# Performance work log

Measured on AMD Instinct MI355X. Metric: run time of the kernel, lower is better.

## Reference

```python
import jax, jax.numpy as jnp
import numpy as np

B, T, C = 4, 2048, 1024
N_HEADS = 16
HEAD_DIM = C // N_HEADS

def setup_inputs() -> dict:
    key = jax.random.key(0)
    k1, k2, k3 = jax.random.split(key, 3)
    x = jax.random.normal(k1, (B, T, C), dtype=jnp.float32)
    w_attn = jax.random.normal(k2, (C, 3 * C), dtype=jnp.float32) * (1.0 / np.sqrt(C))
    b_attn = jnp.zeros((3 * C,), dtype=jnp.float32)
    w_proj = jax.random.normal(k3, (C, C), dtype=jnp.float32) * (1.0 / np.sqrt(C))
    b_proj = jnp.zeros((C,), dtype=jnp.float32)
    return {"x": x, "w_attn": w_attn, "b_attn": b_attn, "w_proj": w_proj, "b_proj": b_proj}

def reference(x, w_attn, b_attn, w_proj, b_proj):
    Bx, Tx, Cx = x.shape
    qkv = x @ w_attn + b_attn                      # [B,T,3C]
    q, k, v = jnp.split(qkv, 3, axis=-1)
    def heads(t):
        return t.reshape(Bx, Tx, N_HEADS, HEAD_DIM).transpose(0, 2, 1, 3)  # [B,H,T,D]
    q, k, v = heads(q), heads(k), heads(v)
    scale = 1.0 / np.sqrt(HEAD_DIM)
    attn = jnp.einsum('bhqd,bhkd->bhqk', q, k) * scale  # [B,H,T,T]
    causal = jnp.tril(jnp.ones((Tx, Tx), dtype=bool))
    attn = jnp.where(causal[None, None, :, :], attn, -jnp.inf)
    attn = jax.nn.softmax(attn, axis=-1)
    out = jnp.einsum('bhqk,bhkd->bhqd', attn, v)        # [B,H,T,D]
    out = out.transpose(0, 2, 1, 3).reshape(Bx, Tx, Cx)
    return out @ w_proj + b_proj
```

## Files before the change

### kernel.cpp

```cpp
#include <hip/hip_runtime.h>
#include <hip/hip_bf16.h>

#define BATCH 4
#define SEQ   2048
#define CH    1024
#define NH    16
#define HD    64
#define BT    8192

typedef __attribute__((ext_vector_type(8))) short bf16x8;
typedef __attribute__((ext_vector_type(4))) float f32x4;
typedef __attribute__((ext_vector_type(16))) float f32x16;

__device__ __forceinline__ unsigned short f2b(float f) {
  __hip_bfloat16 h = __float2bfloat16(f);
  return *reinterpret_cast<unsigned short*>(&h);
}

__device__ __forceinline__ unsigned cvt_pk(float lo, float hi_) {
  unsigned r;
  asm("v_cvt_pk_bf16_f32 %0, %1, %2" : "=v"(r) : "v"(lo), "v"(hi_));
  return r;
}
__device__ __forceinline__ void plane_swap(unsigned &a, unsigned &b) {
  asm("v_permlane32_swap_b32 %0, %1" : "+v"(a), "+v"(b));
}


__global__ void conv_x_bf16(const float* __restrict__ in, unsigned short* __restrict__ out, int n4) {
  int i = blockIdx.x * blockDim.x + threadIdx.x;
  if (i >= n4) return;
  float4 v = reinterpret_cast<const float4*>(in)[i];
  ushort4 o;
  o.x = f2b(v.x); o.y = f2b(v.y); o.z = f2b(v.z); o.w = f2b(v.w);
  reinterpret_cast<ushort4*>(out)[i] = o;
}

__global__ void transpose_w_bf16(const float* __restrict__ in, unsigned short* __restrict__ out,
                                 int R, int Cc) {
  __shared__ float tile[32][33];
  int c0 = blockIdx.x * 32, r0 = blockIdx.y * 32;
  int tx = threadIdx.x, ty = threadIdx.y;
  #pragma unroll
  for (int i = 0; i < 32; i += 8)
    tile[ty + i][tx] = in[(size_t)(r0 + ty + i) * Cc + c0 + tx];
  __syncthreads();
  #pragma unroll
  for (int i = 0; i < 32; i += 8)
    out[(size_t)(c0 + ty + i) * R + r0 + tx] = f2b(tile[tx][ty + i]);
}


#define QSCALE 0.18033688011112042f

#define GSTAGE64(BUF, K0)                                                                      \
  {                                                                                            \
    _Pragma("unroll")                                                                          \
    for (int c = 0; c < 4; ++c) {                                                              \
      int idx = c * 256 + tid;                                                                 \
      int row = idx >> 3;                                                                      \
      int cg = (idx & 7) ^ (row & 7);                                                          \
      const unsigned short* sA = A + (size_t)(m0 + row) * 1024 + (K0) + cg * 8;                \
      __builtin_amdgcn_global_load_lds((const __attribute__((address_space(1))) void*)sA,      \
          (__attribute__((address_space(3))) void*)&sb[(BUF) * 8192 + (c * 256 + (tid & ~63)) * 8], 16, 0, 0); \
      const unsigned short* sB = Bt + (size_t)(n0 + row) * 1024 + (K0) + cg * 8;               \
      __builtin_amdgcn_global_load_lds((const __attribute__((address_space(1))) void*)sB,      \
          (__attribute__((address_space(3))) void*)&sb[16384 + (BUF) * 8192 + (c * 256 + (tid & ~63)) * 8], 16, 0, 0); \
    }                                                                                          \
  }

#define GEMM_MAIN_LOOP                                                                         \
  GSTAGE64(0, 0)                                                                               \
  asm volatile("s_waitcnt vmcnt(0)" ::: "memory");                                             \
  __builtin_amdgcn_s_barrier();                                                                \
  int cur = 0;                                                                                 \
  for (int k0 = 0; k0 < 1024; k0 += 64) {                                                      \
    if (k0 + 64 < 1024) GSTAGE64(cur ^ 1, k0 + 64)                                             \
    _Pragma("unroll")                                                                          \
    for (int sub = 0; sub < 2; ++sub) {                                                        \
      bf16x8 a[4], b[4];                                                                       \
      _Pragma("unroll")                                                                        \
      for (int i = 0; i < 4; ++i) {                                                            \
        int row = wr * 64 + i * 16 + lr;                                                       \
        a[i] = *reinterpret_cast<const bf16x8*>(                                               \
            &sb[cur * 8192 + row * 64 + (((sub * 4 + lh) ^ (lr & 7)) << 3)]);                  \
      }                                                                                        \
      _Pragma("unroll")                                                                        \
      for (int j = 0; j < 4; ++j) {                                                            \
        int row = wc * 64 + j * 16 + lr;                                                       \
        b[j] = *reinterpret_cast<const bf16x8*>(                                               \
            &sb[16384 + cur * 8192 + row * 64 + (((sub * 4 + lh) ^ (lr & 7)) << 3)]);          \
      }                                                                                        \
      _Pragma("unroll")                                                                        \
      for (int i = 0; i < 4; ++i)                                                              \
        _Pragma("unroll")                                                                      \
        for (int j = 0; j < 4; ++j)                                                            \
          acc[i][j] = __builtin_amdgcn_mfma_f32_16x16x32_bf16(a[i], b[j], acc[i][j], 0, 0, 0); \
    }                                                                                          \
    asm volatile("s_waitcnt vmcnt(0)" ::: "memory");                                           \
    __builtin_amdgcn_s_barrier();                                                              \
    cur ^= 1;                                                                                  \
  }

__global__ __launch_bounds__(256) void gemm_qkv(
    const unsigned short* __restrict__ A,
    const unsigned short* __restrict__ Bt,
    const float* __restrict__ bias,
    unsigned short* __restrict__ Qb,
    unsigned short* __restrict__ Kb,
    unsigned short* __restrict__ Vt) {
  __shared__ __align__(16) unsigned short sb[32768];
  int tid = threadIdx.x;
  int lane = tid & 63, wav = tid >> 6;
  int wr = wav >> 1, wc = wav & 1;
  int lr = lane & 15, lh = lane >> 4;
  int m0 = blockIdx.x * 128, n0 = blockIdx.y * 128;

  f32x4 acc[4][4];
  #pragma unroll
  for (int i = 0; i < 4; ++i)
    #pragma unroll
    for (int j = 0; j < 4; ++j)
      acc[i][j] = f32x4{0.f, 0.f, 0.f, 0.f};

  GEMM_MAIN_LOOP

  int which = n0 >> 10;
  int h2 = (n0 >> 6) & 15;
  int bb = m0 >> 11, t0 = m0 & 2047;

  if (which < 2) {
    unsigned short* dst = which ? Kb : Qb;
    float sc = which ? 1.0f : QSCALE;
    size_t headbase = (size_t)(bb * 16 + h2 + wc) * SEQ;
    #pragma unroll
    for (int j = 0; j < 4; ++j) {
      int d = j * 16 + lr;
      float bv = bias[n0 + wc * 64 + d];
      #pragma unroll
      for (int i = 0; i < 4; ++i) {
        #pragma unroll
        for (int r = 0; r < 4; ++r) {
          int t = t0 + wr * 64 + i * 16 + lh * 4 + r;
          dst[(headbase + t) * HD + d] = f2b((acc[i][j][r] + bv) * sc);
        }
      }
    }
  } else {
    unsigned short* tile = sb;
    #pragma unroll
    for (int j = 0; j < 4; ++j) {
      int d = wc * 64 + j * 16 + lr;
      float bv = bias[n0 + d];
      int sw = d & 7;
      #pragma unroll
      for (int i = 0; i < 4; ++i) {
        int cm = wr * 16 + i * 4 + lh;
        unsigned lo = cvt_pk(acc[i][j][0] + bv, acc[i][j][1] + bv);
        unsigned hi_ = cvt_pk(acc[i][j][2] + bv, acc[i][j][3] + bv);
        unsigned long long val = (unsigned long long)lo | ((unsigned long long)hi_ << 32);
        *reinterpret_cast<unsigned long long*>(&tile[d * 128 + ((cm ^ sw) << 2)]) = val;
      }
    }
    __syncthreads();
    #pragma unroll
    for (int it = 0; it < 8; ++it) {
      int pid = it * 256 + tid;
      int drow = pid >> 4, p = pid & 15;
      int sw = drow & 7;
      union { unsigned long long u[2]; bf16x8 v; } u;
      u.u[0] = *reinterpret_cast<const unsigned long long*>(&tile[drow * 128 + (((2 * p) ^ sw) << 2)]);
      u.u[1] = *reinterpret_cast<const unsigned long long*>(&tile[drow * 128 + ((((2 * p) ^ sw) ^ 1) << 2)]);
      *reinterpret_cast<bf16x8*>(
          &Vt[((size_t)(bb * 16 + h2 + (drow >> 6)) * 64 + (drow & 63)) * SEQ + t0 + p * 8]) = u.v;
    }
  }
}


__global__ __launch_bounds__(512, 2) void attn_fwd(
    const unsigned short* __restrict__ Qb,
    const unsigned short* __restrict__ Kb,
    const unsigned short* __restrict__ Vt,
    unsigned short* __restrict__ AO) {
  __shared__ __align__(16) unsigned short sbuf[32768];

  int tid = threadIdx.x;
  int lane = tid & 63, w = tid >> 6;
  int ql = lane & 31, hi = lane >> 5;
  int bid = blockIdx.x;
  int head = bid & 63;
  int qs = 7 - (bid >> 6);
  int q0 = qs * 256;
  int NT = 2 * (qs + 1);
  int b = head >> 4, h = head & 15;

  const unsigned short* Qh = Qb + (size_t)head * SEQ * HD;
  const unsigned short* Kh = Kb + (size_t)head * SEQ * HD;
  const unsigned short* Vh = Vt + (size_t)head * HD * SEQ;

#define STAGE128(BUF, KV0)                                                                     \
  {                                                                                            \
    _Pragma("unroll")                                                                          \
    for (int c = 0; c < 2; ++c) {                                                              \
      int idx = c * 512 + tid;                                                                 \
      int krow = idx >> 3;                                                                     \
      int kcg = (idx & 7) ^ (krow & 7);                                                        \
      const unsigned short* srcK_ = Kh + (size_t)((KV0) + krow) * HD + kcg * 8;                \
      __builtin_amdgcn_global_load_lds((const __attribute__((address_space(1))) void*)srcK_,   \
          (__attribute__((address_space(3))) void*)&sbuf[(BUF) * 8192 + (c * 512 + (tid & ~63)) * 8], 16, 0, 0); \
      int vrow = idx >> 4;                                                                     \
      int vcg = (idx & 15) ^ (vrow & 15);                                                      \
      const unsigned short* srcV_ = Vh + (size_t)vrow * SEQ + (KV0) + vcg * 8;                 \
      __builtin_amdgcn_global_load_lds((const __attribute__((address_space(1))) void*)srcV_,   \
          (__attribute__((address_space(3))) void*)&sbuf[16384 + (BUF) * 8192 + (c * 512 + (tid & ~63)) * 8], 16, 0, 0); \
    }                                                                                          \
  }

  int qg = q0 + w * 32 + ql;
  bf16x8 qf[4];
  #pragma unroll
  for (int dblk = 0; dblk < 4; ++dblk)
    qf[dblk] = *reinterpret_cast<const bf16x8*>(&Qh[(size_t)qg * HD + dblk * 16 + hi * 8]);

  f32x16 o0 = (f32x16)0.0f, o1 = (f32x16)0.0f;
  float mrun = -1e30f, lrun = 0.f;

  STAGE128(0, 0)
  asm volatile("s_waitcnt vmcnt(0)" ::: "memory");
  __builtin_amdgcn_s_barrier();

  int cur = 0;
  int wq_hi = q0 + w * 32 + 31;
  for (int t = 0; t < NT; ++t) {
    int tkv0 = t * 128;
    if (t + 1 < NT) STAGE128(cur ^ 1, tkv0 + 128)

    #pragma unroll
    for (int sub = 0; sub < 2; ++sub) {
      int kv0 = tkv0 + sub * 64;
      if (kv0 <= wq_hi) {
        f32x16 s0 = (f32x16)0.0f, s1 = (f32x16)0.0f;
        int rk0 = sub * 64 + ql, rk1 = sub * 64 + 32 + ql;
        __builtin_amdgcn_s_setprio(1);
        #pragma unroll
        for (int dblk = 0; dblk < 4; ++dblk) {
          bf16x8 kf0 = *reinterpret_cast<const bf16x8*>(
              &sbuf[cur * 8192 + rk0 * 64 + (((dblk * 2 + hi) ^ (rk0 & 7)) << 3)]);
          s0 = __builtin_amdgcn_mfma_f32_32x32x16_bf16(kf0, qf[dblk], s0, 0, 0, 0);
          bf16x8 kf1 = *reinterpret_cast<const bf16x8*>(
              &sbuf[cur * 8192 + rk1 * 64 + (((dblk * 2 + hi) ^ (rk1 & 7)) << 3)]);
          s1 = __builtin_amdgcn_mfma_f32_32x32x16_bf16(kf1, qf[dblk], s1, 0, 0, 0);
        }
        __builtin_amdgcn_s_setprio(0);

        float p[32];
        bool needMask = (kv0 + 63 > q0 + 32 * w);
        #pragma unroll
        for (int r = 0; r < 16; ++r) {
          int cr = (r & 3) + 8 * (r >> 2);
          float v0 = s0[r], v1 = s1[r];
          if (needMask) {
            int kv_ = kv0 + 4 * hi + cr;
            v0 = (kv_ > qg) ? -1e30f : v0;
            v1 = (kv_ + 32 > qg) ? -1e30f : v1;
          }
          p[r] = v0; p[16 + r] = v1;
        }

        float m16[16], m8[8], m4[4], m2[2];
        #pragma unroll
        for (int i = 0; i < 16; ++i) m16[i] = fmaxf(p[i], p[i + 16]);
        #pragma unroll
        for (int i = 0; i < 8; ++i) m8[i] = fmaxf(m16[i], m16[i + 8]);
        #pragma unroll
        for (int i = 0; i < 4; ++i) m4[i] = fmaxf(m8[i], m8[i + 4]);
        m2[0] = fmaxf(m4[0], m4[2]); m2[1] = fmaxf(m4[1], m4[3]);
        float mt = fmaxf(m2[0], m2[1]);
        mt = fmaxf(mt, __shfl_xor(mt, 32));
        float mnew = fmaxf(mrun, mt);
        float alpha = __builtin_amdgcn_exp2f(mrun - mnew);
        mrun = mnew;

        #pragma unroll
        for (int i = 0; i < 32; ++i) p[i] = __builtin_amdgcn_exp2f(p[i] - mnew);
        float a16[16], a8[8], a4[4];
        #pragma unroll
        for (int i = 0; i < 16; ++i) a16[i] = p[i] + p[i + 16];
        #pragma unroll
        for (int i = 0; i < 8; ++i) a8[i] = a16[i] + a16[i + 8];
        #pragma unroll
        for (int i = 0; i < 4; ++i) a4[i] = a8[i] + a8[i + 4];
        float rs = (a4[0] + a4[1]) + (a4[2] + a4[3]);
        rs += __shfl_xor(rs, 32);
        lrun = lrun * alpha + rs;

        #pragma unroll
        for (int i = 0; i < 16; ++i) { o0[i] *= alpha; o1[i] *= alpha; }

        union FU { unsigned u[4]; bf16x8 v; };
        FU fr[4];
        #pragma unroll
        for (int blk = 0; blk < 2; ++blk) {
          unsigned X = cvt_pk(p[blk * 16 + 0], p[blk * 16 + 1]);
          unsigned Z = cvt_pk(p[blk * 16 + 4], p[blk * 16 + 5]);
          plane_swap(X, Z);
          unsigned Y = cvt_pk(p[blk * 16 + 2], p[blk * 16 + 3]);
          unsigned W = cvt_pk(p[blk * 16 + 6], p[blk * 16 + 7]);
          plane_swap(Y, W);
          fr[blk * 2].u[0] = X; fr[blk * 2].u[1] = Y; fr[blk * 2].u[2] = Z; fr[blk * 2].u[3] = W;
          unsigned X2 = cvt_pk(p[blk * 16 + 8], p[blk * 16 + 9]);
          unsigned Z2 = cvt_pk(p[blk * 16 + 12], p[blk * 16 + 13]);
          plane_swap(X2, Z2);
          unsigned Y2 = cvt_pk(p[blk * 16 + 10], p[blk * 16 + 11]);
          unsigned W2 = cvt_pk(p[blk * 16 + 14], p[blk * 16 + 15]);
          plane_swap(Y2, W2);
          fr[blk * 2 + 1].u[0] = X2; fr[blk * 2 + 1].u[1] = Y2;
          fr[blk * 2 + 1].u[2] = Z2; fr[blk * 2 + 1].u[3] = W2;
        }

        __builtin_amdgcn_s_setprio(1);
        #pragma unroll
        for (int kc = 0; kc < 4; ++kc) {
          int rd0 = ql, rd1 = 32 + ql;
          int gch = sub * 8 + (kc << 1) + hi;
          bf16x8 vf0 = *reinterpret_cast<const bf16x8*>(
              &sbuf[16384 + cur * 8192 + rd0 * 128 + ((gch ^ (rd0 & 15)) << 3)]);
          o0 = __builtin_amdgcn_mfma_f32_32x32x16_bf16(vf0, fr[kc].v, o0, 0, 0, 0);
          bf16x8 vf1 = *reinterpret_cast<const bf16x8*>(
              &sbuf[16384 + cur * 8192 + rd1 * 128 + ((gch ^ (rd1 & 15)) << 3)]);
          o1 = __builtin_amdgcn_mfma_f32_32x32x16_bf16(vf1, fr[kc].v, o1, 0, 0, 0);
        }
        __builtin_amdgcn_s_setprio(0);
      }
    }

    asm volatile("s_waitcnt vmcnt(0)" ::: "memory");
    __builtin_amdgcn_s_barrier();
    cur ^= 1;
  }

  float inv = 1.0f / lrun;
  int qloc = w * 32 + ql;
  #pragma unroll
  for (int dblk = 0; dblk < 2; ++dblk) {
    #pragma unroll
    for (int m = 0; m < 4; ++m) {
      float v0, v1, v2, v3;
      if (dblk == 0) {
        v0 = o0[m * 4 + 0] * inv; v1 = o0[m * 4 + 1] * inv;
        v2 = o0[m * 4 + 2] * inv; v3 = o0[m * 4 + 3] * inv;
      } else {
        v0 = o1[m * 4 + 0] * inv; v1 = o1[m * 4 + 1] * inv;
        v2 = o1[m * 4 + 2] * inv; v3 = o1[m * 4 + 3] * inv;
      }
      unsigned u0 = (unsigned)f2b(v0) | ((unsigned)f2b(v1) << 16);
      unsigned u1 = (unsigned)f2b(v2) | ((unsigned)f2b(v3) << 16);
      int slot = (dblk * 4 + m) ^ (qloc & 7);
      unsigned long long val = (unsigned long long)u0 | ((unsigned long long)u1 << 32);
      *reinterpret_cast<unsigned long long*>(&sbuf[qloc * 64 + slot * 8 + hi * 4]) = val;
    }
  }
  __syncthreads();

  #pragma unroll
  for (int it = 0; it < 4; ++it) {
    int qr = it * 64 + (tid >> 3);
    int lc = tid & 7;
    int slot = lc ^ (qr & 7);
    bf16x8 v = *reinterpret_cast<const bf16x8*>(&sbuf[qr * 64 + slot * 8]);
    *reinterpret_cast<bf16x8*>(
        &AO[(size_t)(b * SEQ + q0 + qr) * CH + h * 64 + lc * 8]) = v;
  }
}


__global__ __launch_bounds__(256) void gemm_proj(
    const unsigned short* __restrict__ A,
    const unsigned short* __restrict__ Bt,
    const float* __restrict__ bias,
    float* __restrict__ out) {
  __shared__ __align__(16) unsigned short sb[32768];
  int tid = threadIdx.x;
  int lane = tid & 63, wav = tid >> 6;
  int wr = wav >> 1, wc = wav & 1;
  int lr = lane & 15, lh = lane >> 4;
  int m0 = blockIdx.x * 128, n0 = blockIdx.y * 128;

  f32x4 acc[4][4];
  #pragma unroll
  for (int i = 0; i < 4; ++i)
    #pragma unroll
    for (int j = 0; j < 4; ++j)
      acc[i][j] = f32x4{0.f, 0.f, 0.f, 0.f};

  GEMM_MAIN_LOOP

  #pragma unroll
  for (int i = 0; i < 4; ++i) {
    #pragma unroll
    for (int j = 0; j < 4; ++j) {
      int n = n0 + wc * 64 + j * 16 + lr;
      float bv = bias[n];
      #pragma unroll
      for (int r = 0; r < 4; ++r) {
        int m = m0 + wr * 64 + i * 16 + lh * 4 + r;
        out[(size_t)m * 1024 + n] = acc[i][j][r] + bv;
      }
    }
  }
}


extern "C" void kernel_launch(void* const* d_in, const int* in_sizes, int n_in,
                              void* d_out, int out_size, void* d_ws, size_t ws_size,
                              hipStream_t stream) {
  const float* x      = (const float*)d_in[0];
  const float* w_attn = (const float*)d_in[1];
  const float* b_attn = (const float*)d_in[2];
  const float* w_proj = (const float*)d_in[3];
  const float* b_proj = (const float*)d_in[4];
  float* out = (float*)d_out;

  char* ws = (char*)d_ws;
  unsigned short* xb  = (unsigned short*)(ws);
  unsigned short* wAT = (unsigned short*)(ws + 16777216);
  unsigned short* wPT = (unsigned short*)(ws + 23068672);
  unsigned short* Qb  = (unsigned short*)(ws + 25165824);
  unsigned short* Kb  = (unsigned short*)(ws + 41943040);
  unsigned short* Vt  = (unsigned short*)(ws + 58720256);
  unsigned short* AO  = (unsigned short*)(ws + 75497472);

  conv_x_bf16<<<(BT * CH / 4 + 255) / 256, 256, 0, stream>>>(x, xb, BT * CH / 4);
  transpose_w_bf16<<<dim3(3 * CH / 32, CH / 32), dim3(32, 8), 0, stream>>>(w_attn, wAT, CH, 3 * CH);
  transpose_w_bf16<<<dim3(CH / 32, CH / 32), dim3(32, 8), 0, stream>>>(w_proj, wPT, CH, CH);
  gemm_qkv<<<dim3(BT / 128, 3 * CH / 128), 256, 0, stream>>>(xb, wAT, b_attn, Qb, Kb, Vt);
  attn_fwd<<<512, 512, 0, stream>>>(Qb, Kb, Vt, AO);
  gemm_proj<<<dim3(BT / 128, CH / 128), 256, 0, stream>>>(AO, wPT, b_proj, out);
}
```

Measured before the change: 155.9 us.

## Shrink attention blocks to 128 query rows with 64-wide KV tiles

Re-tiles the flash-attention kernel to 256-thread blocks covering 128 query rows, with 64-key K/V tiles double-buffered in half the shared memory. The grid doubles to 1024 blocks with a 4-blocks-per-CU launch bound, and the V swizzle and output store are adjusted to the narrower tiles. The aim is better load balance across the causal triangle and higher occupancy. In exchange there are more barrier and staging iterations per unit of work, and less K/V reuse per block.

```diff
diff --git a/kernel.cpp b/kernel.cpp
--- a/kernel.cpp
+++ b/kernel.cpp
@@ -178,42 +178,40 @@
 }
 
 
-__global__ __launch_bounds__(512, 2) void attn_fwd(
+__global__ __launch_bounds__(256, 4) void attn_fwd(
     const unsigned short* __restrict__ Qb,
     const unsigned short* __restrict__ Kb,
     const unsigned short* __restrict__ Vt,
     unsigned short* __restrict__ AO) {
-  __shared__ __align__(16) unsigned short sbuf[32768];
+  __shared__ __align__(16) unsigned short sbuf[16384];
 
   int tid = threadIdx.x;
   int lane = tid & 63, w = tid >> 6;
   int ql = lane & 31, hi = lane >> 5;
   int bid = blockIdx.x;
   int head = bid & 63;
-  int qs = 7 - (bid >> 6);
-  int q0 = qs * 256;
-  int NT = 2 * (qs + 1);
+  int qt = 15 - (bid >> 6);
+  int q0 = qt * 128;
+  int NT = 2 * (qt + 1);
   int b = head >> 4, h = head & 15;
 
   const unsigned short* Qh = Qb + (size_t)head * SEQ * HD;
   const unsigned short* Kh = Kb + (size_t)head * SEQ * HD;
   const unsigned short* Vh = Vt + (size_t)head * HD * SEQ;
 
-#define STAGE128(BUF, KV0)                                                                     \
+#define STAGE(BUF, KV0)                                                                        \
   {                                                                                            \
     _Pragma("unroll")                                                                          \
     for (int c = 0; c < 2; ++c) {                                                              \
-      int idx = c * 512 + tid;                                                                 \
-      int krow = idx >> 3;                                                                     \
-      int kcg = (idx & 7) ^ (krow & 7);                                                        \
-      const unsigned short* srcK_ = Kh + (size_t)((KV0) + krow) * HD + kcg * 8;                \
+      int idx = c * 256 + tid;                                                                 \
+      int row = idx >> 3;                                                                      \
+      int cg = (idx & 7) ^ (row & 7);                                                          \
+      const unsigned short* srcK_ = Kh + (size_t)((KV0) + row) * HD + cg * 8;                  \
       __builtin_amdgcn_global_load_lds((const __attribute__((address_space(1))) void*)srcK_,   \
-          (__attribute__((address_space(3))) void*)&sbuf[(BUF) * 8192 + (c * 512 + (tid & ~63)) * 8], 16, 0, 0); \
-      int vrow = idx >> 4;                                                                     \
-      int vcg = (idx & 15) ^ (vrow & 15);                                                      \
-      const unsigned short* srcV_ = Vh + (size_t)vrow * SEQ + (KV0) + vcg * 8;                 \
+          (__attribute__((address_space(3))) void*)&sbuf[(BUF) * 4096 + (c * 256 + (tid & ~63)) * 8], 16, 0, 0); \
+      const unsigned short* srcV_ = Vh + (size_t)row * SEQ + (KV0) + cg * 8;                   \
       __builtin_amdgcn_global_load_lds((const __attribute__((address_space(1))) void*)srcV_,   \
-          (__attribute__((address_space(3))) void*)&sbuf[16384 + (BUF) * 8192 + (c * 512 + (tid & ~63)) * 8], 16, 0, 0); \
+          (__attribute__((address_space(3))) void*)&sbuf[8192 + (BUF) * 4096 + (c * 256 + (tid & ~63)) * 8], 16, 0, 0); \
     }                                                                                          \
   }
 
@@ -226,113 +224,108 @@
   f32x16 o0 = (f32x16)0.0f, o1 = (f32x16)0.0f;
   float mrun = -1e30f, lrun = 0.f;
 
-  STAGE128(0, 0)
+  STAGE(0, 0)
   asm volatile("s_waitcnt vmcnt(0)" ::: "memory");
   __builtin_amdgcn_s_barrier();
 
   int cur = 0;
   int wq_hi = q0 + w * 32 + 31;
   for (int t = 0; t < NT; ++t) {
-    int tkv0 = t * 128;
-    if (t + 1 < NT) STAGE128(cur ^ 1, tkv0 + 128)
-
-    #pragma unroll
-    for (int sub = 0; sub < 2; ++sub) {
-      int kv0 = tkv0 + sub * 64;
-      if (kv0 <= wq_hi) {
-        f32x16 s0 = (f32x16)0.0f, s1 = (f32x16)0.0f;
-        int rk0 = sub * 64 + ql, rk1 = sub * 64 + 32 + ql;
-        __builtin_amdgcn_s_setprio(1);
-        #pragma unroll
-        for (int dblk = 0; dblk < 4; ++dblk) {
-          bf16x8 kf0 = *reinterpret_cast<const bf16x8*>(
-              &sbuf[cur * 8192 + rk0 * 64 + (((dblk * 2 + hi) ^ (rk0 & 7)) << 3)]);
-          s0 = __builtin_amdgcn_mfma_f32_32x32x16_bf16(kf0, qf[dblk], s0, 0, 0, 0);
-          bf16x8 kf1 = *reinterpret_cast<const bf16x8*>(
-              &sbuf[cur * 8192 + rk1 * 64 + (((dblk * 2 + hi) ^ (rk1 & 7)) << 3)]);
-          s1 = __builtin_amdgcn_mfma_f32_32x32x16_bf16(kf1, qf[dblk], s1, 0, 0, 0);
+    int kv0 = t * 64;
+    if (t + 1 < NT) STAGE(cur ^ 1, kv0 + 64)
+
+    if (kv0 <= wq_hi) {
+      f32x16 s0 = (f32x16)0.0f, s1 = (f32x16)0.0f;
+      int rk0 = ql, rk1 = 32 + ql;
+      __builtin_amdgcn_s_setprio(1);
+      #pragma unroll
+      for (int dblk = 0; dblk < 4; ++dblk) {
+        bf16x8 kf0 = *reinterpret_cast<const bf16x8*>(
+            &sbuf[cur * 4096 + rk0 * 64 + (((dblk * 2 + hi) ^ (rk0 & 7)) << 3)]);
+        s0 = __builtin_amdgcn_mfma_f32_32x32x16_bf16(kf0, qf[dblk], s0, 0, 0, 0);
+        bf16x8 kf1 = *reinterpret_cast<const bf16x8*>(
+            &sbuf[cur * 4096 + rk1 * 64 + (((dblk * 2 + hi) ^ (rk1 & 7)) << 3)]);
+        s1 = __builtin_amdgcn_mfma_f32_32x32x16_bf16(kf1, qf[dblk], s1, 0, 0, 0);
+      }
+      __builtin_amdgcn_s_setprio(0);
+
+      float p[32];
+      bool needMask = (kv0 + 63 > q0 + 32 * w);
+      #pragma unroll
+      for (int r = 0; r < 16; ++r) {
+        int cr = (r & 3) + 8 * (r >> 2);
+        float v0 = s0[r], v1 = s1[r];
+        if (needMask) {
+          int kv_ = kv0 + 4 * hi + cr;
+          v0 = (kv_ > qg) ? -1e30f : v0;
+          v1 = (kv_ + 32 > qg) ? -1e30f : v1;
         }
-        __builtin_amdgcn_s_setprio(0);
-
-        float p[32];
-        bool needMask = (kv0 + 63 > q0 + 32 * w);
-        #pragma unroll
-        for (int r = 0; r < 16; ++r) {
-          int cr = (r & 3) + 8 * (r >> 2);
-          float v0 = s0[r], v1 = s1[r];
-          if (needMask) {
-            int kv_ = kv0 + 4 * hi + cr;
-            v0 = (kv_ > qg) ? -1e30f : v0;
-            v1 = (kv_ + 32 > qg) ? -1e30f : v1;
-          }
-          p[r] = v0; p[16 + r] = v1;
-        }
-
-        float m16[16], m8[8], m4[4], m2[2];
-        #pragma unroll
-        for (int i = 0; i < 16; ++i) m16[i] = fmaxf(p[i], p[i + 16]);
-        #pragma unroll
-        for (int i = 0; i < 8; ++i) m8[i] = fmaxf(m16[i], m16[i + 8]);
-        #pragma unroll
-        for (int i = 0; i < 4; ++i) m4[i] = fmaxf(m8[i], m8[i + 4]);
-        m2[0] = fmaxf(m4[0], m4[2]); m2[1] = fmaxf(m4[1], m4[3]);
-        float mt = fmaxf(m2[0], m2[1]);
-        mt = fmaxf(mt, __shfl_xor(mt, 32));
-        float mnew = fmaxf(mrun, mt);
-        float alpha = __builtin_amdgcn_exp2f(mrun - mnew);
-        mrun = mnew;
-
-        #pragma unroll
-        for (int i = 0; i < 32; ++i) p[i] = __builtin_amdgcn_exp2f(p[i] - mnew);
-        float a16[16], a8[8], a4[4];
-        #pragma unroll
-        for (int i = 0; i < 16; ++i) a16[i] = p[i] + p[i + 16];
-        #pragma unroll
-        for (int i = 0; i < 8; ++i) a8[i] = a16[i] + a16[i + 8];
-        #pragma unroll
-        for (int i = 0; i < 4; ++i) a4[i] = a8[i] + a8[i + 4];
-        float rs = (a4[0] + a4[1]) + (a4[2] + a4[3]);
-        rs += __shfl_xor(rs, 32);
-        lrun = lrun * alpha + rs;
-
-        #pragma unroll
-        for (int i = 0; i < 16; ++i) { o0[i] *= alpha; o1[i] *= alpha; }
-
-        union FU { unsigned u[4]; bf16x8 v; };
-        FU fr[4];
-        #pragma unroll
-        for (int blk = 0; blk < 2; ++blk) {
-          unsigned X = cvt_pk(p[blk * 16 + 0], p[blk * 16 + 1]);
-          unsigned Z = cvt_pk(p[blk * 16 + 4], p[blk * 16 + 5]);
-          plane_swap(X, Z);
-          unsigned Y = cvt_pk(p[blk * 16 + 2], p[blk * 16 + 3]);
-          unsigned W = cvt_pk(p[blk * 16 + 6], p[blk * 16 + 7]);
-          plane_swap(Y, W);
-          fr[blk * 2].u[0] = X; fr[blk * 2].u[1] = Y; fr[blk * 2].u[2] = Z; fr[blk * 2].u[3] = W;
-          unsigned X2 = cvt_pk(p[blk * 16 + 8], p[blk * 16 + 9]);
-          unsigned Z2 = cvt_pk(p[blk * 16 + 12], p[blk * 16 + 13]);
-          plane_swap(X2, Z2);
-          unsigned Y2 = cvt_pk(p[blk * 16 + 10], p[blk * 16 + 11]);
-          unsigned W2 = cvt_pk(p[blk * 16 + 14], p[blk * 16 + 15]);
-          plane_swap(Y2, W2);
-          fr[blk * 2 + 1].u[0] = X2; fr[blk * 2 + 1].u[1] = Y2;
-          fr[blk * 2 + 1].u[2] = Z2; fr[blk * 2 + 1].u[3] = W2;
-        }
-
-        __builtin_amdgcn_s_setprio(1);
-        #pragma unroll
-        for (int kc = 0; kc < 4; ++kc) {
-          int rd0 = ql, rd1 = 32 + ql;
-          int gch = sub * 8 + (kc << 1) + hi;
-          bf16x8 vf0 = *reinterpret_cast<const bf16x8*>(
-              &sbuf[16384 + cur * 8192 + rd0 * 128 + ((gch ^ (rd0 & 15)) << 3)]);
-          o0 = __builtin_amdgcn_mfma_f32_32x32x16_bf16(vf0, fr[kc].v, o0, 0, 0, 0);
-          bf16x8 vf1 = *reinterpret_cast<const bf16x8*>(
-              &sbuf[16384 + cur * 8192 + rd1 * 128 + ((gch ^ (rd1 & 15)) << 3)]);
-          o1 = __builtin_amdgcn_mfma_f32_32x32x16_bf16(vf1, fr[kc].v, o1, 0, 0, 0);
-        }
-        __builtin_amdgcn_s_setprio(0);
-      }
+        p[r] = v0; p[16 + r] = v1;
+      }
+
+      float m16[16], m8[8], m4[4], m2[2];
+      #pragma unroll
+      for (int i = 0; i < 16; ++i) m16[i] = fmaxf(p[i], p[i + 16]);
+      #pragma unroll
+      for (int i = 0; i < 8; ++i) m8[i] = fmaxf(m16[i], m16[i + 8]);
+      #pragma unroll
+      for (int i = 0; i < 4; ++i) m4[i] = fmaxf(m8[i], m8[i + 4]);
+      m2[0] = fmaxf(m4[0], m4[2]); m2[1] = fmaxf(m4[1], m4[3]);
+      float mt = fmaxf(m2[0], m2[1]);
+      mt = fmaxf(mt, __shfl_xor(mt, 32));
+      float mnew = fmaxf(mrun, mt);
+      float alpha = __builtin_amdgcn_exp2f(mrun - mnew);
+      mrun = mnew;
+
+      #pragma unroll
+      for (int i = 0; i < 32; ++i) p[i] = __builtin_amdgcn_exp2f(p[i] - mnew);
+      float a16[16], a8[8], a4[4];
+      #pragma unroll
+      for (int i = 0; i < 16; ++i) a16[i] = p[i] + p[i + 16];
+      #pragma unroll
+      for (int i = 0; i < 8; ++i) a8[i] = a16[i] + a16[i + 8];
+      #pragma unroll
+      for (int i = 0; i < 4; ++i) a4[i] = a8[i] + a8[i + 4];
+      float rs = (a4[0] + a4[1]) + (a4[2] + a4[3]);
+      rs += __shfl_xor(rs, 32);
+      lrun = lrun * alpha + rs;
+
+      #pragma unroll
+      for (int i = 0; i < 16; ++i) { o0[i] *= alpha; o1[i] *= alpha; }
+
+      union FU { unsigned u[4]; bf16x8 v; };
+      FU fr[4];
+      #pragma unroll
+      for (int blk = 0; blk < 2; ++blk) {
+        unsigned X = cvt_pk(p[blk * 16 + 0], p[blk * 16 + 1]);
+        unsigned Z = cvt_pk(p[blk * 16 + 4], p[blk * 16 + 5]);
+        plane_swap(X, Z);
+        unsigned Y = cvt_pk(p[blk * 16 + 2], p[blk * 16 + 3]);
+        unsigned W = cvt_pk(p[blk * 16 + 6], p[blk * 16 + 7]);
+        plane_swap(Y, W);
+        fr[blk * 2].u[0] = X; fr[blk * 2].u[1] = Y; fr[blk * 2].u[2] = Z; fr[blk * 2].u[3] = W;
+        unsigned X2 = cvt_pk(p[blk * 16 + 8], p[blk * 16 + 9]);
+        unsigned Z2 = cvt_pk(p[blk * 16 + 12], p[blk * 16 + 13]);
+        plane_swap(X2, Z2);
+        unsigned Y2 = cvt_pk(p[blk * 16 + 10], p[blk * 16 + 11]);
+        unsigned W2 = cvt_pk(p[blk * 16 + 14], p[blk * 16 + 15]);
+        plane_swap(Y2, W2);
+        fr[blk * 2 + 1].u[0] = X2; fr[blk * 2 + 1].u[1] = Y2;
+        fr[blk * 2 + 1].u[2] = Z2; fr[blk * 2 + 1].u[3] = W2;
+      }
+
+      __builtin_amdgcn_s_setprio(1);
+      #pragma unroll
+      for (int kc = 0; kc < 4; ++kc) {
+        int rd0 = ql, rd1 = 32 + ql;
+        bf16x8 vf0 = *reinterpret_cast<const bf16x8*>(
+            &sbuf[8192 + cur * 4096 + rd0 * 64 + ((((kc << 1) + hi) ^ (rd0 & 7)) << 3)]);
+        o0 = __builtin_amdgcn_mfma_f32_32x32x16_bf16(vf0, fr[kc].v, o0, 0, 0, 0);
+        bf16x8 vf1 = *reinterpret_cast<const bf16x8*>(
+            &sbuf[8192 + cur * 4096 + rd1 * 64 + ((((kc << 1) + hi) ^ (rd1 & 7)) << 3)]);
+        o1 = __builtin_amdgcn_mfma_f32_32x32x16_bf16(vf1, fr[kc].v, o1, 0, 0, 0);
+      }
+      __builtin_amdgcn_s_setprio(0);
     }
 
     asm volatile("s_waitcnt vmcnt(0)" ::: "memory");
@@ -365,7 +358,7 @@
 
   #pragma unroll
   for (int it = 0; it < 4; ++it) {
-    int qr = it * 64 + (tid >> 3);
+    int qr = it * 32 + (tid >> 3);
     int lc = tid & 7;
     int slot = lc ^ (qr & 7);
     bf16x8 v = *reinterpret_cast<const bf16x8*>(&sbuf[qr * 64 + slot * 8]);
@@ -435,6 +428,6 @@
   transpose_w_bf16<<<dim3(3 * CH / 32, CH / 32), dim3(32, 8), 0, stream>>>(w_attn, wAT, CH, 3 * CH);
   transpose_w_bf16<<<dim3(CH / 32, CH / 32), dim3(32, 8), 0, stream>>>(w_proj, wPT, CH, CH);
   gemm_qkv<<<dim3(BT / 128, 3 * CH / 128), 256, 0, stream>>>(xb, wAT, b_attn, Qb, Kb, Vt);
-  attn_fwd<<<512, 512, 0, stream>>>(Qb, Kb, Vt, AO);
+  attn_fwd<<<1024, 256, 0, stream>>>(Qb, Kb, Vt, AO);
   gemm_proj<<<dim3(BT / 128, CH / 128), 256, 0, stream>>>(AO, wPT, b_proj, out);
 }
```

New measurement: 160.7 us. 3.1% more time.
